# Performance work log

Hardware: AMD Instinct MI355X
Metric: run time of the kernel (lower is better)

## Reference

```python
import jax, jax.numpy as jnp
import numpy as np

B, S, DIN, DOUT = 4, 2048, 4096, 4096
W_SCALE = 64.0   # makes round(weight*scale) produce non-trivial int8 values
X_SCALE = 16.0   # input_scale so x*scale truncates to non-zero int32 values


def setup_inputs() -> dict:
    key = jax.random.key(0)
    k1, k2, k3 = jax.random.split(key, 3)
    # kaiming_uniform fan_in: bound = sqrt(6/fan_in)
    bound = float(np.sqrt(6.0 / DIN))
    weight = jax.random.uniform(k1, (DOUT, DIN), jnp.float32, -bound, bound)
    x = jax.random.normal(k2, (B, S, DIN), jnp.float32)
    bias = jax.random.normal(k3, (DOUT,), jnp.float32) * 0.01
    weight_scale = jnp.full((DOUT,), W_SCALE, jnp.float32)
    input_scale = jnp.full((1,), X_SCALE, jnp.float32)
    return {"x": x, "weight": weight, "bias": bias,
            "weight_scale": weight_scale, "input_scale": input_scale}


def reference(x, weight, bias, weight_scale, input_scale):
    # x = x * input_scale (pre-scale path of forward)
    xs = x * input_scale
    # fake-quant weights: round to int8 with wraparound, like torch .to(int8)
    w_int = jnp.round(weight * weight_scale[:, None]).astype(jnp.int8)
    # x.to(torch.int32): truncation toward zero
    x_int = xs.astype(jnp.int32)
    # F.linear on the integer-valued tensors (computed in f32: values are exact ints)
    acc = jnp.einsum('bsd,od->bso', x_int.astype(jnp.float32),
                     w_int.astype(jnp.float32))
    acc = acc + bias  # bias added inside linear
    # dequant: divide by per-channel weight_scale and the scalar input_scale
    out = acc / (weight_scale * input_scale)
    return out
```

## Files before the change

kernel.cpp:

```cpp
#include <hip/hip_runtime.h>

#define GM 8192
#define GN 4096
#define GK 4096

#define BM 128
#define BN 256
#define BK 64
#define NTILE (GK / BK)
#define ABYTES (BM * BK)
#define TILE_LDS (ABYTES + BN * BK)

using int4v = __attribute__((ext_vector_type(4))) int;

__global__ __launch_bounds__(256) void quant_xw_k(
    const float4* __restrict__ x, unsigned int* __restrict__ xq,
    const float4* __restrict__ w, unsigned int* __restrict__ wq,
    const float* __restrict__ wscale, const float* __restrict__ iscale,
    int n4x, int n4tot) {
    const float xs = *iscale;
    const int stride = gridDim.x * blockDim.x;
    for (int i = blockIdx.x * blockDim.x + threadIdx.x; i < n4tot; i += stride) {
        if (i < n4x) {
            float4 v = x[i];
            int q0 = (int)(v.x * xs);
            int q1 = (int)(v.y * xs);
            int q2 = (int)(v.z * xs);
            int q3 = (int)(v.w * xs);
            xq[i] = (unsigned int)(q0 & 0xff)
                  | ((unsigned int)(q1 & 0xff) << 8)
                  | ((unsigned int)(q2 & 0xff) << 16)
                  | ((unsigned int)(q3 & 0xff) << 24);
        } else {
            int j = i - n4x;
            float s = wscale[j >> 10];
            float4 v = w[j];
            int q0 = (int)rintf(v.x * s);
            int q1 = (int)rintf(v.y * s);
            int q2 = (int)rintf(v.z * s);
            int q3 = (int)rintf(v.w * s);
            wq[j] = (unsigned int)(q0 & 0xff)
                  | ((unsigned int)(q1 & 0xff) << 8)
                  | ((unsigned int)(q2 & 0xff) << 16)
                  | ((unsigned int)(q3 & 0xff) << 24);
        }
    }
}

__global__ __launch_bounds__(512, 4) void qlinear_gemm_i8(
    const signed char* __restrict__ Aq,
    const signed char* __restrict__ Bq,
    const float* __restrict__ bias,
    const float* __restrict__ wscale,
    const float* __restrict__ iscale,
    float* __restrict__ C) {
    __shared__ signed char smem[3 * TILE_LDS];

    const int tid  = threadIdx.x;
    const int wave = tid >> 6;
    const int lane = tid & 63;
    const int m0 = blockIdx.x * BM;
    const int n0 = blockIdx.y * BN;
    const int wm = (wave >> 2) * 64;
    const int wn = (wave & 3) * 64;

    int4v acc[4][4];
#pragma unroll
    for (int i = 0; i < 4; ++i)
#pragma unroll
        for (int j = 0; j < 4; ++j)
            acc[i][j] = int4v{0, 0, 0, 0};

    const int kc = ((tid & 3) ^ ((tid >> 3) & 3)) * 16;
    const signed char* gA = Aq + (size_t)(m0 + (tid >> 2)) * GK + kc;
    const signed char* gB = Bq + (size_t)(n0 + (tid >> 2)) * GK + kc;
    const int dst = tid * 16;

    const int pos = (((lane >> 4) ^ ((lane >> 1) & 3))) * 16;
    const int fAo = (wm + (lane & 15)) * BK + pos;
    const int fBo = ABYTES + (wn + (lane & 15)) * BK + pos;

#define GLL16(g, l)                                                     \
    __builtin_amdgcn_global_load_lds(                                   \
        (__attribute__((address_space(1))) void*)(void*)(g),            \
        (__attribute__((address_space(3))) void*)(void*)(l), 16, 0, 0)

#define STAGE(kb, soff)                                                 \
    do {                                                                \
        GLL16(gA + (kb), smem + (soff) + dst);                          \
        GLL16(gB + (kb), smem + (soff) + ABYTES + dst);                 \
        GLL16(gB + (size_t)128 * GK + (kb),                             \
              smem + (soff) + ABYTES + 8192 + dst);                     \
    } while (0)

    STAGE(0, 0);
    STAGE(BK, TILE_LDS);
    asm volatile("s_waitcnt vmcnt(3)" ::: "memory");
    __builtin_amdgcn_s_barrier();
    __builtin_amdgcn_sched_barrier(0);

    int bc = 0;
    int bn2 = TILE_LDS;
    int bs = 2 * TILE_LDS;
    int kst = 2 * BK;
    for (int t = 0; t < NTILE; ++t) {
        STAGE(kst, bs);
        __builtin_amdgcn_sched_barrier(0);

        const signed char* fA = smem + bc + fAo;
        const signed char* fB = smem + bc + fBo;
        int4v a[4], b[4];
#pragma unroll
        for (int i = 0; i < 4; ++i)
            a[i] = *(const int4v*)(fA + i * 1024);
#pragma unroll
        for (int j = 0; j < 4; ++j)
            b[j] = *(const int4v*)(fB + j * 1024);

        __builtin_amdgcn_s_setprio(1);
#pragma unroll
        for (int mi = 0; mi < 4; ++mi)
#pragma unroll
            for (int ni = 0; ni < 4; ++ni)
                acc[mi][ni] = __builtin_amdgcn_mfma_i32_16x16x64_i8(
                    a[mi], b[ni], acc[mi][ni], 0, 0, 0);
        __builtin_amdgcn_s_setprio(0);

        asm volatile("s_waitcnt vmcnt(3)" ::: "memory");
        __builtin_amdgcn_s_barrier();
        __builtin_amdgcn_sched_barrier(0);

        int tmp = bc; bc = bn2; bn2 = bs; bs = tmp;
        kst += BK; if (kst >= GK) kst = 0;
    }

    const float isc = *iscale;
#pragma unroll
    for (int ni = 0; ni < 4; ++ni) {
        const int col = n0 + wn + ni * 16 + (lane & 15);
        const float bs_ = bias[col];
        const float inv = 1.0f / (wscale[col] * isc);
#pragma unroll
        for (int mi = 0; mi < 4; ++mi) {
            const int row0 = m0 + wm + mi * 16 + (lane >> 4) * 4;
#pragma unroll
            for (int r = 0; r < 4; ++r) {
                C[(size_t)(row0 + r) * GN + col] =
                    ((float)acc[mi][ni][r] + bs_) * inv;
            }
        }
    }
#undef STAGE
#undef GLL16
}

extern "C" void kernel_launch(void* const* d_in, const int* in_sizes, int n_in,
                              void* d_out, int out_size, void* d_ws, size_t ws_size,
                              hipStream_t stream) {
    const float* x      = (const float*)d_in[0];
    const float* w      = (const float*)d_in[1];
    const float* bias   = (const float*)d_in[2];
    const float* wscale = (const float*)d_in[3];
    const float* iscale = (const float*)d_in[4];
    float* out = (float*)d_out;

    signed char* xq = (signed char*)d_ws;
    signed char* wq = xq + (size_t)GM * GK;

    const int n4x = GM * GK / 4;
    const int n4w = GN * GK / 4;
    quant_xw_k<<<3072, 256, 0, stream>>>((const float4*)x, (unsigned int*)xq,
                                         (const float4*)w, (unsigned int*)wq,
                                         wscale, iscale, n4x, n4x + n4w);

    dim3 grid(GM / BM, GN / BN);
    qlinear_gemm_i8<<<grid, 512, 0, stream>>>(xq, wq, bias, wscale, iscale, out);
}
```

Baseline: 404.3 us.

## Enlarge GEMM tile to 256x256 with phased double-buffered LDS pipeline

Doubles the block tile along M to 256x256, so each wave computes a 128x64 sub-tile with 32 accumulators. This doubles operand reuse per LDS byte and halves global traffic per output. The three-stage LDS ring is replaced by two 32 KB slots. Each K-tile is split into four barrier-separated phases that interleave A-fragment LDS reads with MFMA groups while the next tile streams in. The cost is more registers, occupancy limited to two blocks per CU, and many extra barriers per K step.

```diff
diff --git a/kernel.cpp b/kernel.cpp
--- a/kernel.cpp
+++ b/kernel.cpp
@@ -4,12 +4,11 @@
 #define GN 4096
 #define GK 4096
 
-#define BM 128
+#define BM 256
 #define BN 256
 #define BK 64
 #define NTILE (GK / BK)
-#define ABYTES (BM * BK)
-#define TILE_LDS (ABYTES + BN * BK)
+#define SLOT 32768
 
 using int4v = __attribute__((ext_vector_type(4))) int;
 
@@ -47,38 +46,40 @@
     }
 }
 
-__global__ __launch_bounds__(512, 4) void qlinear_gemm_i8(
+__global__ __launch_bounds__(512, 2) void qlinear_gemm_i8(
     const signed char* __restrict__ Aq,
     const signed char* __restrict__ Bq,
     const float* __restrict__ bias,
     const float* __restrict__ wscale,
     const float* __restrict__ iscale,
     float* __restrict__ C) {
-    __shared__ signed char smem[3 * TILE_LDS];
+    __shared__ signed char smem[2 * SLOT];
 
     const int tid  = threadIdx.x;
     const int wave = tid >> 6;
     const int lane = tid & 63;
     const int m0 = blockIdx.x * BM;
     const int n0 = blockIdx.y * BN;
-    const int wm = (wave >> 2) * 64;
+    const int wm = (wave >> 2) * 128;
     const int wn = (wave & 3) * 64;
 
-    int4v acc[4][4];
+    int4v acc[8][4];
 #pragma unroll
-    for (int i = 0; i < 4; ++i)
+    for (int i = 0; i < 8; ++i)
 #pragma unroll
         for (int j = 0; j < 4; ++j)
             acc[i][j] = int4v{0, 0, 0, 0};
 
     const int kc = ((tid & 3) ^ ((tid >> 3) & 3)) * 16;
-    const signed char* gA = Aq + (size_t)(m0 + (tid >> 2)) * GK + kc;
-    const signed char* gB = Bq + (size_t)(n0 + (tid >> 2)) * GK + kc;
+    const signed char* gA  = Aq + (size_t)(m0 + (tid >> 2)) * GK + kc;
+    const signed char* gA2 = gA + (size_t)128 * GK;
+    const signed char* gB  = Bq + (size_t)(n0 + (tid >> 2)) * GK + kc;
+    const signed char* gB2 = gB + (size_t)128 * GK;
     const int dst = tid * 16;
 
     const int pos = (((lane >> 4) ^ ((lane >> 1) & 3))) * 16;
-    const int fAo = (wm + (lane & 15)) * BK + pos;
-    const int fBo = ABYTES + (wn + (lane & 15)) * BK + pos;
+    const int fAo = (wm + (lane & 15)) * 64 + pos;
+    const int fBo = 16384 + (wn + (lane & 15)) * 64 + pos;
 
 #define GLL16(g, l)                                                     \
     __builtin_amdgcn_global_load_lds(                                   \
@@ -87,51 +88,64 @@
 
 #define STAGE(kb, soff)                                                 \
     do {                                                                \
-        GLL16(gA + (kb), smem + (soff) + dst);                          \
-        GLL16(gB + (kb), smem + (soff) + ABYTES + dst);                 \
-        GLL16(gB + (size_t)128 * GK + (kb),                             \
-              smem + (soff) + ABYTES + 8192 + dst);                     \
+        GLL16(gA  + (kb), smem + (soff) + dst);                         \
+        GLL16(gA2 + (kb), smem + (soff) + 8192 + dst);                  \
+        GLL16(gB  + (kb), smem + (soff) + 16384 + dst);                 \
+        GLL16(gB2 + (kb), smem + (soff) + 24576 + dst);                 \
+    } while (0)
+
+#define DSR(off) (*(const int4v*)(smem + (off)))
+#define MFMA(A, B, Cc) __builtin_amdgcn_mfma_i32_16x16x64_i8(A, B, Cc, 0, 0, 0)
+
+#define PH(q)                                                           \
+    __builtin_amdgcn_s_barrier();                                       \
+    asm volatile("s_waitcnt lgkmcnt(0)" ::: "memory");                  \
+    __builtin_amdgcn_sched_barrier(0);                                  \
+    __builtin_amdgcn_s_setprio(1);                                      \
+    acc[2*(q)  ][0] = MFMA(pa0, bfr0, acc[2*(q)  ][0]);                 \
+    acc[2*(q)+1][0] = MFMA(pa1, bfr0, acc[2*(q)+1][0]);                 \
+    acc[2*(q)  ][1] = MFMA(pa0, bfr1, acc[2*(q)  ][1]);                 \
+    acc[2*(q)+1][1] = MFMA(pa1, bfr1, acc[2*(q)+1][1]);                 \
+    acc[2*(q)  ][2] = MFMA(pa0, bfr2, acc[2*(q)  ][2]);                 \
+    acc[2*(q)+1][2] = MFMA(pa1, bfr2, acc[2*(q)+1][2]);                 \
+    acc[2*(q)  ][3] = MFMA(pa0, bfr3, acc[2*(q)  ][3]);                 \
+    acc[2*(q)+1][3] = MFMA(pa1, bfr3, acc[2*(q)+1][3]);                 \
+    __builtin_amdgcn_s_setprio(0);                                      \
+    __builtin_amdgcn_s_barrier();
+
+#define HALF(SOFF, STAGE_CODE)                                          \
+    do {                                                                \
+        STAGE_CODE;                                                     \
+        bfr0 = DSR((SOFF) + fBo);                                       \
+        bfr1 = DSR((SOFF) + fBo + 1024);                                \
+        bfr2 = DSR((SOFF) + fBo + 2048);                                \
+        bfr3 = DSR((SOFF) + fBo + 3072);                                \
+        pa0  = DSR((SOFF) + fAo);                                       \
+        pa1  = DSR((SOFF) + fAo + 1024);                                \
+        PH(0)                                                           \
+        pa0 = DSR((SOFF) + fAo + 2048);                                 \
+        pa1 = DSR((SOFF) + fAo + 3072);                                 \
+        PH(1)                                                           \
+        pa0 = DSR((SOFF) + fAo + 4096);                                 \
+        pa1 = DSR((SOFF) + fAo + 5120);                                 \
+        PH(2)                                                           \
+        pa0 = DSR((SOFF) + fAo + 6144);                                 \
+        pa1 = DSR((SOFF) + fAo + 7168);                                 \
+        asm volatile("s_waitcnt vmcnt(0)" ::: "memory");                \
+        PH(3)                                                           \
     } while (0)
 
     STAGE(0, 0);
-    STAGE(BK, TILE_LDS);
-    asm volatile("s_waitcnt vmcnt(3)" ::: "memory");
+    asm volatile("s_waitcnt vmcnt(0)" ::: "memory");
     __builtin_amdgcn_s_barrier();
     __builtin_amdgcn_sched_barrier(0);
 
-    int bc = 0;
-    int bn2 = TILE_LDS;
-    int bs = 2 * TILE_LDS;
-    int kst = 2 * BK;
-    for (int t = 0; t < NTILE; ++t) {
-        STAGE(kst, bs);
-        __builtin_amdgcn_sched_barrier(0);
-
-        const signed char* fA = smem + bc + fAo;
-        const signed char* fB = smem + bc + fBo;
-        int4v a[4], b[4];
-#pragma unroll
-        for (int i = 0; i < 4; ++i)
-            a[i] = *(const int4v*)(fA + i * 1024);
-#pragma unroll
-        for (int j = 0; j < 4; ++j)
-            b[j] = *(const int4v*)(fB + j * 1024);
-
-        __builtin_amdgcn_s_setprio(1);
-#pragma unroll
-        for (int mi = 0; mi < 4; ++mi)
-#pragma unroll
-            for (int ni = 0; ni < 4; ++ni)
-                acc[mi][ni] = __builtin_amdgcn_mfma_i32_16x16x64_i8(
-                    a[mi], b[ni], acc[mi][ni], 0, 0, 0);
-        __builtin_amdgcn_s_setprio(0);
-
-        asm volatile("s_waitcnt vmcnt(3)" ::: "memory");
-        __builtin_amdgcn_s_barrier();
-        __builtin_amdgcn_sched_barrier(0);
-
-        int tmp = bc; bc = bn2; bn2 = bs; bs = tmp;
-        kst += BK; if (kst >= GK) kst = 0;
+    int4v bfr0, bfr1, bfr2, bfr3, pa0, pa1;
+    int kA = BK;
+    int kB = 2 * BK;
+    for (int it = 0; it < NTILE / 2; ++it) {
+        HALF(0,    { STAGE(kA, SLOT); kA += 2 * BK; });
+        HALF(SLOT, { if (kB < GK) { STAGE(kB, 0); kB += 2 * BK; } });
     }
 
     const float isc = *iscale;
@@ -141,7 +155,7 @@
         const float bs_ = bias[col];
         const float inv = 1.0f / (wscale[col] * isc);
 #pragma unroll
-        for (int mi = 0; mi < 4; ++mi) {
+        for (int mi = 0; mi < 8; ++mi) {
             const int row0 = m0 + wm + mi * 16 + (lane >> 4) * 4;
 #pragma unroll
             for (int r = 0; r < 4; ++r) {
@@ -150,6 +164,10 @@
             }
         }
     }
+#undef HALF
+#undef PH
+#undef DSR
+#undef MFMA
 #undef STAGE
 #undef GLL16
 }
```

Result: no change. 411.7 us (+1.8%).
